# Kernel optimization log

Hardware: AMD Instinct MI355X
Metric: run time of the kernel (lower is better)

## Reference

```python
import jax, jax.numpy as jnp
import numpy as np

D_MODEL = 1024
NUM_HEADS = 16
HEAD_DIM = D_MODEL // NUM_HEADS


def setup_inputs() -> dict:
    key = jax.random.key(0)
    ks = jax.random.split(key, 11)
    B, S = 2, 2048
    s = 1.0 / np.sqrt(D_MODEL)
    inp = {
        "query": jax.random.normal(ks[0], (B, S, D_MODEL), jnp.float32),
        "key": jax.random.normal(ks[1], (B, S, D_MODEL), jnp.float32),
        "value": jax.random.normal(ks[2], (B, S, D_MODEL), jnp.float32),
        "Wq": jax.random.normal(ks[3], (D_MODEL, D_MODEL), jnp.float32) * s,
        "bq": jnp.zeros((D_MODEL,), jnp.float32),
        "Wk": jax.random.normal(ks[4], (D_MODEL, D_MODEL), jnp.float32) * s,
        "bk": jnp.zeros((D_MODEL,), jnp.float32),
        "Wv": jax.random.normal(ks[5], (D_MODEL, D_MODEL), jnp.float32) * s,
        "bv": jnp.zeros((D_MODEL,), jnp.float32),
        "Wo": jax.random.normal(ks[6], (D_MODEL, D_MODEL), jnp.float32) * s,
        "bo": jnp.zeros((D_MODEL,), jnp.float32),
    }
    return inp


def _split_heads(x):
    B, S, _ = x.shape
    return x.reshape(B, S, NUM_HEADS, HEAD_DIM).transpose(0, 2, 1, 3)  # [B,H,S,d]


def reference(query, key, value, Wq, bq, Wk, bk, Wv, bv, Wo, bo):
    Q = _split_heads(query @ Wq.T + bq)
    K = _split_heads(key @ Wk.T + bk)
    V = _split_heads(value @ Wv.T + bv)
    scale = 1.0 / jnp.sqrt(jnp.asarray(HEAD_DIM, jnp.float32))
    scores = jnp.einsum("bhqd,bhkd->bhqk", Q, K) * scale  # [B,H,S,S]
    weights = jax.nn.softmax(scores, axis=-1)
    attn = jnp.einsum("bhqk,bhkd->bhqd", weights, V)
    B, H, S, d = attn.shape
    attn = attn.transpose(0, 2, 1, 3).reshape(B, S, H * d)
    return attn @ Wo.T + bo
```

## Files before the change

### kernel.cpp

```cpp
#include <hip/hip_runtime.h>


typedef unsigned short u16;
typedef __attribute__((ext_vector_type(8))) short short8;
typedef __attribute__((ext_vector_type(4))) float floatx4;

__device__ __forceinline__ float bf2f(u16 x) {
  return __uint_as_float(((unsigned)x) << 16);
}
__device__ __forceinline__ u16 f2bf(float f) {
  unsigned x = __float_as_uint(f);
  return (u16)((x + 0x7fffu + ((x >> 16) & 1u)) >> 16);
}
__device__ __forceinline__ void gll16(const u16* g, u16* lds) {
  __builtin_amdgcn_global_load_lds((const __attribute__((address_space(1))) void*)g,
                                   (__attribute__((address_space(3))) void*)lds,
                                   16, 0, 0);
}

__global__ __launch_bounds__(256) void cvt_kernel(
    const float* __restrict__ q, const float* __restrict__ k, const float* __restrict__ v,
    const float* __restrict__ wq, const float* __restrict__ wk,
    const float* __restrict__ wv, const float* __restrict__ wo,
    const float* __restrict__ bq, const float* __restrict__ bk,
    const float* __restrict__ bv, const float* __restrict__ bo,
    u16* __restrict__ ws) {
  const int i4 = (blockIdx.x * 256 + threadIdx.x) * 4;
  const float* src;
  u16* dst;
  int local;
  if (i4 < 4194304)        { src = q;  dst = ws;            local = i4; }
  else if (i4 < 8388608)   { src = k;  dst = ws + 4194304;  local = i4 - 4194304; }
  else if (i4 < 12582912)  { src = v;  dst = ws + 8388608;  local = i4 - 8388608; }
  else if (i4 < 13631488)  { src = wq; dst = ws + 12582912; local = i4 - 12582912; }
  else if (i4 < 14680064)  { src = wk; dst = ws + 13631488; local = i4 - 13631488; }
  else if (i4 < 15728640)  { src = wv; dst = ws + 14680064; local = i4 - 14680064; }
  else if (i4 < 16777216)  { src = wo; dst = ws + 15728640; local = i4 - 15728640; }
  else if (i4 < 16778240)  { src = bq; dst = ws + 16777216; local = i4 - 16777216; }
  else if (i4 < 16779264)  { src = bk; dst = ws + 16779264; local = i4 - 16778240; }
  else if (i4 < 16780288)  { src = bv; dst = ws + 16781312; local = i4 - 16779264; }
  else                     { src = bo; dst = ws + 16783360; local = i4 - 16780288; }
  const float4 f = *(const float4*)(src + local);
  ushort4 o;
  o.x = f2bf(f.x); o.y = f2bf(f.y); o.z = f2bf(f.z); o.w = f2bf(f.w);
  *(ushort4*)(dst + local) = o;
}

__device__ __forceinline__ void gemm_tile(
    const u16* __restrict__ X, const u16* __restrict__ W,
    const u16* __restrict__ bias, u16* __restrict__ out16, float* __restrict__ out32,
    int row0, int col0, int mode, float oscale, u16* As, u16* Bs) {
  const int tid = threadIdx.x;
  const int w = tid >> 6, l = tid & 63;
  const int lan = l & 15, quad = l >> 4;
  const int wm = w & 1, wn = w >> 1;

  floatx4 acc[4][4];
#pragma unroll
  for (int i = 0; i < 4; ++i)
#pragma unroll
    for (int j = 0; j < 4; ++j) acc[i][j] = (floatx4)0.0f;

  const int r0 = tid >> 2, kq0 = tid & 3;
  const int r1 = (tid + 256) >> 2;
  u16* aB0 = As + w * 512;
  u16* aB1 = As + 2048 + w * 512;
  u16* bB0 = Bs + w * 512;
  u16* bB1 = Bs + 2048 + w * 512;
  const u16* Xa0 = X + (size_t)(row0 + r0) * 1024 + kq0 * 8;
  const u16* Xa1 = X + (size_t)(row0 + r1) * 1024 + kq0 * 8;
  const u16* Wb0 = W + (size_t)(col0 + r0) * 1024 + kq0 * 8;
  const u16* Wb1 = W + (size_t)(col0 + r1) * 1024 + kq0 * 8;

  for (int kt = 0; kt < 32; ++kt) {
    gll16(Xa0 + kt * 32, aB0);
    gll16(Xa1 + kt * 32, aB1);
    gll16(Wb0 + kt * 32, bB0);
    gll16(Wb1 + kt * 32, bB1);
    __syncthreads();

    short8 af[4], bfr[4];
#pragma unroll
    for (int i = 0; i < 4; ++i)
      af[i] = *(const short8*)(As + (wm * 64 + i * 16 + lan) * 32 + quad * 8);
#pragma unroll
    for (int j = 0; j < 4; ++j)
      bfr[j] = *(const short8*)(Bs + (wn * 64 + j * 16 + lan) * 32 + quad * 8);
#pragma unroll
    for (int i = 0; i < 4; ++i)
#pragma unroll
      for (int j = 0; j < 4; ++j)
        acc[i][j] = __builtin_amdgcn_mfma_f32_16x16x32_bf16(af[i], bfr[j], acc[i][j], 0, 0, 0);
    __syncthreads();
  }

#pragma unroll
  for (int i = 0; i < 4; ++i) {
    const int mb = row0 + wm * 64 + i * 16 + quad * 4;
#pragma unroll
    for (int j = 0; j < 4; ++j) {
      const int n = col0 + wn * 64 + j * 16 + lan;
      const float bv = bf2f(bias[n]);
      if (mode == 0) {
#pragma unroll
        for (int r = 0; r < 4; ++r)
          out16[(size_t)(mb + r) * 1024 + n] = f2bf((acc[i][j][r] + bv) * oscale);
      } else if (mode == 1) {
        const int b = mb >> 11, s = mb & 2047;
        const int h = n >> 6, dd = n & 63;
        ushort4 v;
        v.x = f2bf(acc[i][j][0] + bv);
        v.y = f2bf(acc[i][j][1] + bv);
        v.z = f2bf(acc[i][j][2] + bv);
        v.w = f2bf(acc[i][j][3] + bv);
        *(ushort4*)(out16 + (size_t)((b * 16 + h) * 64 + dd) * 2048 + s) = v;
      } else {
#pragma unroll
        for (int r = 0; r < 4; ++r)
          out32[(size_t)(mb + r) * 1024 + n] = acc[i][j][r] + bv;
      }
    }
  }
}

__global__ __launch_bounds__(256) void qkv_kernel(
    const u16* __restrict__ xq, const u16* __restrict__ xk, const u16* __restrict__ xv,
    const u16* __restrict__ Wq, const u16* __restrict__ Wk, const u16* __restrict__ Wv,
    const u16* __restrict__ bq, const u16* __restrict__ bk, const u16* __restrict__ bv,
    u16* __restrict__ Qo, u16* __restrict__ Ko, u16* __restrict__ Vto) {
  __shared__ __align__(16) u16 As[128 * 32];
  __shared__ __align__(16) u16 Bs[128 * 32];
  const int bx = blockIdx.x;
  const int tile_m = bx / 24;
  const int rem = bx - tile_m * 24;
  const int which = rem >> 3;
  const int col0 = (rem & 7) * 128;
  const u16* X = which == 0 ? xq : (which == 1 ? xk : xv);
  const u16* W = which == 0 ? Wq : (which == 1 ? Wk : Wv);
  const u16* bias = which == 0 ? bq : (which == 1 ? bk : bv);
  u16* out = which == 0 ? Qo : (which == 1 ? Ko : Vto);
  const float C = 0.125f * 1.4426950408889634f;
  gemm_tile(X, W, bias, out, nullptr, tile_m * 128, col0, which == 2 ? 1 : 0,
            which == 0 ? C : 1.0f, As, Bs);
}

__global__ __launch_bounds__(256) void proj_kernel(
    const u16* __restrict__ X, const u16* __restrict__ W,
    const u16* __restrict__ bias, float* __restrict__ out) {
  __shared__ __align__(16) u16 As[128 * 32];
  __shared__ __align__(16) u16 Bs[128 * 32];
  const int bx = blockIdx.x;
  gemm_tile(X, W, bias, nullptr, out, (bx >> 3) * 128, (bx & 7) * 128, 2, 1.0f, As, Bs);
}

#define PAD 72
#define FIXMAX 16.0f
__global__ __launch_bounds__(256, 4) void attn_kernel(
    const u16* __restrict__ Q, const u16* __restrict__ K,
    const u16* __restrict__ Vt, u16* __restrict__ O) {
  __shared__ __align__(16) u16 Qs[64 * PAD];
  __shared__ __align__(16) u16 Ks[64 * PAD];
  __shared__ __align__(16) u16 Vs[64 * PAD];
  __shared__ __align__(16) u16 Ps[64 * PAD];
  const int tid = threadIdx.x;
  const int w = tid >> 6, l = tid & 63;
  const int lan = l & 15, quad = l >> 4;
  const int q0 = blockIdx.x * 64;
  const int bh = blockIdx.y;
  const int b = bh >> 4, h = bh & 15;
  const u16* Qg = Q + (size_t)(b * 2048 + q0) * 1024 + h * 64;
  const u16* Kg = K + (size_t)(b * 2048) * 1024 + h * 64;
  const u16* Vg = Vt + (size_t)((b * 16 + h) * 64) * 2048;

  {
    const int c0 = tid, c1 = tid + 256;
    *(short8*)(Qs + (c0 >> 3) * PAD + (c0 & 7) * 8) =
        *(const short8*)(Qg + (size_t)(c0 >> 3) * 1024 + (c0 & 7) * 8);
    *(short8*)(Qs + (c1 >> 3) * PAD + (c1 & 7) * 8) =
        *(const short8*)(Qg + (size_t)(c1 >> 3) * 1024 + (c1 & 7) * 8);
  }
  __syncthreads();

  short8 aq[2];
#pragma unroll
  for (int kk = 0; kk < 2; ++kk)
    aq[kk] = *(const short8*)(Qs + (w * 16 + lan) * PAD + kk * 32 + quad * 8);

  float lrun[4];
  floatx4 oacc[4];
#pragma unroll
  for (int r = 0; r < 4; ++r) lrun[r] = 0.f;
#pragma unroll
  for (int nd = 0; nd < 4; ++nd) oacc[nd] = (floatx4)0.0f;

  const int rowA = tid >> 3, colq = tid & 7;
  const int rowB = (tid + 256) >> 3;

  short8 k0 = *(const short8*)(Kg + (size_t)rowA * 1024 + colq * 8);
  short8 k1 = *(const short8*)(Kg + (size_t)rowB * 1024 + colq * 8);
  short8 v0 = *(const short8*)(Vg + (size_t)rowA * 2048 + colq * 8);
  short8 v1 = *(const short8*)(Vg + (size_t)rowB * 2048 + colq * 8);

  for (int kt = 0; kt < 32; ++kt) {
    __syncthreads();
    *(short8*)(Ks + rowA * PAD + colq * 8) = k0;
    *(short8*)(Ks + rowB * PAD + colq * 8) = k1;
    *(short8*)(Vs + rowA * PAD + colq * 8) = v0;
    *(short8*)(Vs + rowB * PAD + colq * 8) = v1;
    __syncthreads();

    const int kn = kt < 31 ? kt + 1 : 31;
    k0 = *(const short8*)(Kg + (size_t)(kn * 64 + rowA) * 1024 + colq * 8);
    k1 = *(const short8*)(Kg + (size_t)(kn * 64 + rowB) * 1024 + colq * 8);
    v0 = *(const short8*)(Vg + (size_t)rowA * 2048 + kn * 64 + colq * 8);
    v1 = *(const short8*)(Vg + (size_t)rowB * 2048 + kn * 64 + colq * 8);

    short8 bkf[4][2], vb[4][2];
#pragma unroll
    for (int nj = 0; nj < 4; ++nj)
#pragma unroll
      for (int kk = 0; kk < 2; ++kk)
        bkf[nj][kk] = *(const short8*)(Ks + (nj * 16 + lan) * PAD + kk * 32 + quad * 8);
#pragma unroll
    for (int nd = 0; nd < 4; ++nd)
#pragma unroll
      for (int kk = 0; kk < 2; ++kk)
        vb[nd][kk] = *(const short8*)(Vs + (nd * 16 + lan) * PAD + kk * 32 + quad * 8);

    floatx4 sacc[4];
#pragma unroll
    for (int nj = 0; nj < 4; ++nj) sacc[nj] = (floatx4)(-FIXMAX);
#pragma unroll
    for (int kk = 0; kk < 2; ++kk)
#pragma unroll
      for (int nj = 0; nj < 4; ++nj)
        sacc[nj] = __builtin_amdgcn_mfma_f32_16x16x32_bf16(aq[kk], bkf[nj][kk], sacc[nj], 0, 0, 0);

#pragma unroll
    for (int r = 0; r < 4; ++r) {
      const float p0 = exp2f(sacc[0][r]), p1 = exp2f(sacc[1][r]);
      const float p2 = exp2f(sacc[2][r]), p3 = exp2f(sacc[3][r]);
      lrun[r] += (p0 + p1) + (p2 + p3);
      const int qrow = w * 16 + quad * 4 + r;
      Ps[qrow * PAD + lan] = f2bf(p0);
      Ps[qrow * PAD + 16 + lan] = f2bf(p1);
      Ps[qrow * PAD + 32 + lan] = f2bf(p2);
      Ps[qrow * PAD + 48 + lan] = f2bf(p3);
    }
    __threadfence_block();

    short8 pa[2];
#pragma unroll
    for (int kk = 0; kk < 2; ++kk)
      pa[kk] = *(const short8*)(Ps + (w * 16 + lan) * PAD + kk * 32 + quad * 8);
#pragma unroll
    for (int kk = 0; kk < 2; ++kk)
#pragma unroll
      for (int nd = 0; nd < 4; ++nd)
        oacc[nd] = __builtin_amdgcn_mfma_f32_16x16x32_bf16(pa[kk], vb[nd][kk], oacc[nd], 0, 0, 0);
  }

#pragma unroll
  for (int r = 0; r < 4; ++r) {
    float ls = lrun[r];
#pragma unroll
    for (int d = 1; d < 16; d <<= 1) ls += __shfl_xor(ls, d);
    const float inv = 1.0f / ls;
    const int mg = b * 2048 + q0 + w * 16 + quad * 4 + r;
#pragma unroll
    for (int nd = 0; nd < 4; ++nd) {
      const int col = h * 64 + nd * 16 + lan;
      O[(size_t)mg * 1024 + col] = f2bf(oacc[nd][r] * inv);
    }
  }
}

extern "C" void kernel_launch(void* const* d_in, const int* in_sizes, int n_in,
                              void* d_out, int out_size, void* d_ws, size_t ws_size,
                              hipStream_t stream) {
  const float* query = (const float*)d_in[0];
  const float* key_ = (const float*)d_in[1];
  const float* value = (const float*)d_in[2];
  const float* Wq = (const float*)d_in[3];
  const float* bq = (const float*)d_in[4];
  const float* Wk = (const float*)d_in[5];
  const float* bk = (const float*)d_in[6];
  const float* Wv = (const float*)d_in[7];
  const float* bv = (const float*)d_in[8];
  const float* Wo = (const float*)d_in[9];
  const float* bo = (const float*)d_in[10];
  float* out = (float*)d_out;

  u16* ws = (u16*)d_ws;
  u16* Xq = ws;
  u16* Xk = ws + 4194304;
  u16* Xv = ws + 8388608;
  u16* cWq = ws + 12582912;
  u16* cWk = ws + 13631488;
  u16* cWv = ws + 14680064;
  u16* cWo = ws + 15728640;
  u16* cbq = ws + 16777216;
  u16* cbk = ws + 16779264;
  u16* cbv = ws + 16781312;
  u16* cbo = ws + 16783360;
  u16* Qw = ws + 17301504;
  u16* Kw = ws + 21495808;
  u16* Vtw = ws + 25690112;
  u16* Ow = ws + 29884416;

  cvt_kernel<<<16388, 256, 0, stream>>>(query, key_, value, Wq, Wk, Wv, Wo,
                                        bq, bk, bv, bo, ws);
  qkv_kernel<<<768, 256, 0, stream>>>(Xq, Xk, Xv, cWq, cWk, cWv, cbq, cbk, cbv,
                                      Qw, Kw, Vtw);
  attn_kernel<<<dim3(32, 32), 256, 0, stream>>>(Qw, Kw, Vtw, Ow);
  proj_kernel<<<256, 256, 0, stream>>>(Ow, cWo, cbo, out);
}
```

Before: 270.0 us.

## Split attention key range across waves with per-wave LDS and cross-wave reduction

Each of the four waves now handles all 64 query rows against its own quarter of the keys, instead of each wave owning 16 query rows over all keys. K, V and P tiles live in per-wave LDS regions, so the block-wide barriers inside the loop become wave-local waitcnt fences. The row sums and output accumulators are reduced across waves through LDS at the end. This removes per-iteration block synchronisation and redundant K/V fragment loads, but it raises register use (occupancy hint lowered from 4 to 2) and adds an epilogue reduction.

```diff
diff --git a/kernel.cpp b/kernel.cpp
--- a/kernel.cpp
+++ b/kernel.cpp
@@ -17,6 +17,7 @@
                                    (__attribute__((address_space(3))) void*)lds,
                                    16, 0, 0);
 }
+#define DSFENCE() __asm__ volatile("s_waitcnt lgkmcnt(0)" ::: "memory")
 
 __global__ __launch_bounds__(256) void cvt_kernel(
     const float* __restrict__ q, const float* __restrict__ k, const float* __restrict__ v,
@@ -153,15 +154,12 @@
   gemm_tile(X, W, bias, nullptr, out, (bx >> 3) * 128, (bx & 7) * 128, 2, 1.0f, As, Bs);
 }
 
-#define PAD 72
 #define FIXMAX 16.0f
-__global__ __launch_bounds__(256, 4) void attn_kernel(
+__global__ __launch_bounds__(256, 2) void attn_kernel(
     const u16* __restrict__ Q, const u16* __restrict__ K,
     const u16* __restrict__ Vt, u16* __restrict__ O) {
-  __shared__ __align__(16) u16 Qs[64 * PAD];
-  __shared__ __align__(16) u16 Ks[64 * PAD];
-  __shared__ __align__(16) u16 Vs[64 * PAD];
-  __shared__ __align__(16) u16 Ps[64 * PAD];
+  __shared__ __align__(16) u16 lds[30208];
+  __shared__ float Lbuf[256];
   const int tid = threadIdx.x;
   const int w = tid >> 6, l = tid & 63;
   const int lan = l & 15, quad = l >> 4;
@@ -169,109 +167,134 @@
   const int bh = blockIdx.y;
   const int b = bh >> 4, h = bh & 15;
   const u16* Qg = Q + (size_t)(b * 2048 + q0) * 1024 + h * 64;
-  const u16* Kg = K + (size_t)(b * 2048) * 1024 + h * 64;
-  const u16* Vg = Vt + (size_t)((b * 16 + h) * 64) * 2048;
-
-  {
-    const int c0 = tid, c1 = tid + 256;
-    *(short8*)(Qs + (c0 >> 3) * PAD + (c0 & 7) * 8) =
-        *(const short8*)(Qg + (size_t)(c0 >> 3) * 1024 + (c0 & 7) * 8);
-    *(short8*)(Qs + (c1 >> 3) * PAD + (c1 & 7) * 8) =
-        *(const short8*)(Qg + (size_t)(c1 >> 3) * 1024 + (c1 & 7) * 8);
-  }
+  const u16* Kg = K + (size_t)(b * 2048 + w * 512) * 1024 + h * 64;
+  const u16* Vg = Vt + (size_t)((b * 16 + h) * 64) * 2048 + w * 512;
+  u16* Ksw = lds + w * 2304;
+  u16* Vsw = lds + 9216 + w * 2560;
+  u16* Psw = lds + 19456 + w * 2560;
+
+  short8 aq[4][2];
+#pragma unroll
+  for (int mi = 0; mi < 4; ++mi)
+#pragma unroll
+    for (int kk = 0; kk < 2; ++kk)
+      aq[mi][kk] = *(const short8*)(Qg + (size_t)(mi * 16 + lan) * 1024 + kk * 32 + quad * 8);
+
+  float lrun[4][4];
+  floatx4 oacc[4][4];
+#pragma unroll
+  for (int mi = 0; mi < 4; ++mi) {
+#pragma unroll
+    for (int r = 0; r < 4; ++r) lrun[mi][r] = 0.f;
+#pragma unroll
+    for (int nd = 0; nd < 4; ++nd) oacc[mi][nd] = (floatx4)0.0f;
+  }
+
+  const int krow = l >> 3, kcol = (l & 7) * 8;
+  const int vdd = l >> 2, vcol = (l & 3) * 8;
+
+  short8 kp[4], vp[4];
+#pragma unroll
+  for (int p = 0; p < 4; ++p) {
+    kp[p] = *(const short8*)(Kg + (size_t)(p * 8 + krow) * 1024 + kcol);
+    vp[p] = *(const short8*)(Vg + (size_t)(p * 16 + vdd) * 2048 + vcol);
+  }
+
+  for (int kt = 0; kt < 16; ++kt) {
+    DSFENCE();
+#pragma unroll
+    for (int p = 0; p < 4; ++p) {
+      *(short8*)(Ksw + (p * 8 + krow) * 72 + kcol) = kp[p];
+      *(short8*)(Vsw + (p * 16 + vdd) * 40 + vcol) = vp[p];
+    }
+    DSFENCE();
+
+    const int kn = kt < 15 ? kt + 1 : 15;
+#pragma unroll
+    for (int p = 0; p < 4; ++p) {
+      kp[p] = *(const short8*)(Kg + (size_t)(kn * 32 + p * 8 + krow) * 1024 + kcol);
+      vp[p] = *(const short8*)(Vg + (size_t)(p * 16 + vdd) * 2048 + kn * 32 + vcol);
+    }
+
+    short8 bkf[2][2];
+#pragma unroll
+    for (int nj = 0; nj < 2; ++nj)
+#pragma unroll
+      for (int kk = 0; kk < 2; ++kk)
+        bkf[nj][kk] = *(const short8*)(Ksw + (nj * 16 + lan) * 72 + kk * 32 + quad * 8);
+    floatx4 sacc[4][2];
+#pragma unroll
+    for (int mi = 0; mi < 4; ++mi)
+#pragma unroll
+      for (int nj = 0; nj < 2; ++nj) sacc[mi][nj] = (floatx4)(-FIXMAX);
+#pragma unroll
+    for (int kk = 0; kk < 2; ++kk)
+#pragma unroll
+      for (int mi = 0; mi < 4; ++mi)
+#pragma unroll
+        for (int nj = 0; nj < 2; ++nj)
+          sacc[mi][nj] =
+              __builtin_amdgcn_mfma_f32_16x16x32_bf16(aq[mi][kk], bkf[nj][kk], sacc[mi][nj], 0, 0, 0);
+
+#pragma unroll
+    for (int mi = 0; mi < 4; ++mi)
+#pragma unroll
+      for (int r = 0; r < 4; ++r) {
+        const float p0 = exp2f(sacc[mi][0][r]);
+        const float p1 = exp2f(sacc[mi][1][r]);
+        lrun[mi][r] += p0 + p1;
+        const int qrow = mi * 16 + quad * 4 + r;
+        Psw[qrow * 40 + lan] = f2bf(p0);
+        Psw[qrow * 40 + 16 + lan] = f2bf(p1);
+      }
+    DSFENCE();
+
+    short8 pa[4], vb[4];
+#pragma unroll
+    for (int mi = 0; mi < 4; ++mi)
+      pa[mi] = *(const short8*)(Psw + (mi * 16 + lan) * 40 + quad * 8);
+#pragma unroll
+    for (int nd = 0; nd < 4; ++nd)
+      vb[nd] = *(const short8*)(Vsw + (nd * 16 + lan) * 40 + quad * 8);
+#pragma unroll
+    for (int mi = 0; mi < 4; ++mi)
+#pragma unroll
+      for (int nd = 0; nd < 4; ++nd)
+        oacc[mi][nd] = __builtin_amdgcn_mfma_f32_16x16x32_bf16(pa[mi], vb[nd], oacc[mi][nd], 0, 0, 0);
+  }
+
+#pragma unroll
+  for (int mi = 0; mi < 4; ++mi)
+#pragma unroll
+    for (int r = 0; r < 4; ++r) {
+      float ls = lrun[mi][r];
+#pragma unroll
+      for (int d = 1; d < 16; d <<= 1) ls += __shfl_xor(ls, d);
+      if (lan == 0) Lbuf[w * 64 + mi * 16 + quad * 4 + r] = ls;
+    }
   __syncthreads();
-
-  short8 aq[2];
-#pragma unroll
-  for (int kk = 0; kk < 2; ++kk)
-    aq[kk] = *(const short8*)(Qs + (w * 16 + lan) * PAD + kk * 32 + quad * 8);
-
-  float lrun[4];
-  floatx4 oacc[4];
-#pragma unroll
-  for (int r = 0; r < 4; ++r) lrun[r] = 0.f;
-#pragma unroll
-  for (int nd = 0; nd < 4; ++nd) oacc[nd] = (floatx4)0.0f;
-
-  const int rowA = tid >> 3, colq = tid & 7;
-  const int rowB = (tid + 256) >> 3;
-
-  short8 k0 = *(const short8*)(Kg + (size_t)rowA * 1024 + colq * 8);
-  short8 k1 = *(const short8*)(Kg + (size_t)rowB * 1024 + colq * 8);
-  short8 v0 = *(const short8*)(Vg + (size_t)rowA * 2048 + colq * 8);
-  short8 v1 = *(const short8*)(Vg + (size_t)rowB * 2048 + colq * 8);
-
-  for (int kt = 0; kt < 32; ++kt) {
+  const int qm = tid >> 2, d0 = (tid & 3) * 4;
+  const float linv =
+      1.0f / (Lbuf[qm] + Lbuf[64 + qm] + Lbuf[128 + qm] + Lbuf[192 + qm]);
+  float* Obuf = (float*)(lds + 19456);
+
+#pragma unroll
+  for (int nd = 0; nd < 4; ++nd) {
     __syncthreads();
-    *(short8*)(Ks + rowA * PAD + colq * 8) = k0;
-    *(short8*)(Ks + rowB * PAD + colq * 8) = k1;
-    *(short8*)(Vs + rowA * PAD + colq * 8) = v0;
-    *(short8*)(Vs + rowB * PAD + colq * 8) = v1;
+#pragma unroll
+    for (int mi = 0; mi < 4; ++mi)
+#pragma unroll
+      for (int r = 0; r < 4; ++r)
+        Obuf[w * 1088 + (mi * 16 + quad * 4 + r) * 17 + lan] = oacc[mi][nd][r];
     __syncthreads();
-
-    const int kn = kt < 31 ? kt + 1 : 31;
-    k0 = *(const short8*)(Kg + (size_t)(kn * 64 + rowA) * 1024 + colq * 8);
-    k1 = *(const short8*)(Kg + (size_t)(kn * 64 + rowB) * 1024 + colq * 8);
-    v0 = *(const short8*)(Vg + (size_t)rowA * 2048 + kn * 64 + colq * 8);
-    v1 = *(const short8*)(Vg + (size_t)rowB * 2048 + kn * 64 + colq * 8);
-
-    short8 bkf[4][2], vb[4][2];
-#pragma unroll
-    for (int nj = 0; nj < 4; ++nj)
-#pragma unroll
-      for (int kk = 0; kk < 2; ++kk)
-        bkf[nj][kk] = *(const short8*)(Ks + (nj * 16 + lan) * PAD + kk * 32 + quad * 8);
-#pragma unroll
-    for (int nd = 0; nd < 4; ++nd)
-#pragma unroll
-      for (int kk = 0; kk < 2; ++kk)
-        vb[nd][kk] = *(const short8*)(Vs + (nd * 16 + lan) * PAD + kk * 32 + quad * 8);
-
-    floatx4 sacc[4];
-#pragma unroll
-    for (int nj = 0; nj < 4; ++nj) sacc[nj] = (floatx4)(-FIXMAX);
-#pragma unroll
-    for (int kk = 0; kk < 2; ++kk)
-#pragma unroll
-      for (int nj = 0; nj < 4; ++nj)
-        sacc[nj] = __builtin_amdgcn_mfma_f32_16x16x32_bf16(aq[kk], bkf[nj][kk], sacc[nj], 0, 0, 0);
-
-#pragma unroll
-    for (int r = 0; r < 4; ++r) {
-      const float p0 = exp2f(sacc[0][r]), p1 = exp2f(sacc[1][r]);
-      const float p2 = exp2f(sacc[2][r]), p3 = exp2f(sacc[3][r]);
-      lrun[r] += (p0 + p1) + (p2 + p3);
-      const int qrow = w * 16 + quad * 4 + r;
-      Ps[qrow * PAD + lan] = f2bf(p0);
-      Ps[qrow * PAD + 16 + lan] = f2bf(p1);
-      Ps[qrow * PAD + 32 + lan] = f2bf(p2);
-      Ps[qrow * PAD + 48 + lan] = f2bf(p3);
-    }
-    __threadfence_block();
-
-    short8 pa[2];
-#pragma unroll
-    for (int kk = 0; kk < 2; ++kk)
-      pa[kk] = *(const short8*)(Ps + (w * 16 + lan) * PAD + kk * 32 + quad * 8);
-#pragma unroll
-    for (int kk = 0; kk < 2; ++kk)
-#pragma unroll
-      for (int nd = 0; nd < 4; ++nd)
-        oacc[nd] = __builtin_amdgcn_mfma_f32_16x16x32_bf16(pa[kk], vb[nd][kk], oacc[nd], 0, 0, 0);
-  }
-
-#pragma unroll
-  for (int r = 0; r < 4; ++r) {
-    float ls = lrun[r];
-#pragma unroll
-    for (int d = 1; d < 16; d <<= 1) ls += __shfl_xor(ls, d);
-    const float inv = 1.0f / ls;
-    const int mg = b * 2048 + q0 + w * 16 + quad * 4 + r;
-#pragma unroll
-    for (int nd = 0; nd < 4; ++nd) {
-      const int col = h * 64 + nd * 16 + lan;
-      O[(size_t)mg * 1024 + col] = f2bf(oacc[nd][r] * inv);
-    }
+    ushort4 ov;
+#pragma unroll
+    for (int e = 0; e < 4; ++e) {
+      const float s = Obuf[qm * 17 + d0 + e] + Obuf[1088 + qm * 17 + d0 + e] +
+                      Obuf[2176 + qm * 17 + d0 + e] + Obuf[3264 + qm * 17 + d0 + e];
+      ((u16*)&ov)[e] = f2bf(s * linv);
+    }
+    *(ushort4*)(O + (size_t)(b * 2048 + q0 + qm) * 1024 + h * 64 + nd * 16 + d0) = ov;
   }
 }
 
```

New measurement: 273.1 us. Within noise of the previous version (+1.1%).

## Load V and Q fragments directly from global, drop their LDS staging

Applied to the files above, without the earlier changes.

The attention kernel now reads Q fragments and V^T MFMA operands straight from global memory into registers, so the Qs and Vs shared buffers and the V LDS store/load path are removed. K staging in LDS is kept. It also switches to a native exp2 builtin, packs bf16 conversions in pairs, replaces the block fence with an explicit lgkmcnt wait, and lowers the launch-bounds occupancy hint from 4 to 3. This cuts LDS traffic and footprint, but V reads become uncoalesced per-lane global loads issued without prefetch ahead of use, which adds latency.

```diff
diff --git a/kernel.cpp b/kernel.cpp
--- a/kernel.cpp
+++ b/kernel.cpp
@@ -1,4 +1,5 @@
 #include <hip/hip_runtime.h>
+#include <hip/hip_bf16.h>
 
 
 typedef unsigned short u16;
@@ -12,11 +13,23 @@
   unsigned x = __float_as_uint(f);
   return (u16)((x + 0x7fffu + ((x >> 16) & 1u)) >> 16);
 }
+__device__ __forceinline__ ushort2 pk_bf16(float a, float b) {
+  __hip_bfloat162 h2 = __float22bfloat162_rn(make_float2(a, b));
+  ushort2 u;
+  __builtin_memcpy(&u, &h2, 4);
+  return u;
+}
+#if __has_builtin(__builtin_amdgcn_exp2f)
+#define EXP2(x) __builtin_amdgcn_exp2f(x)
+#else
+#define EXP2(x) exp2f(x)
+#endif
 __device__ __forceinline__ void gll16(const u16* g, u16* lds) {
   __builtin_amdgcn_global_load_lds((const __attribute__((address_space(1))) void*)g,
                                    (__attribute__((address_space(3))) void*)lds,
                                    16, 0, 0);
 }
+#define DSFENCE() __asm__ volatile("s_waitcnt lgkmcnt(0)" ::: "memory")
 
 __global__ __launch_bounds__(256) void cvt_kernel(
     const float* __restrict__ q, const float* __restrict__ k, const float* __restrict__ v,
@@ -153,15 +166,14 @@
   gemm_tile(X, W, bias, nullptr, out, (bx >> 3) * 128, (bx & 7) * 128, 2, 1.0f, As, Bs);
 }
 
-#define PAD 72
 #define FIXMAX 16.0f
-__global__ __launch_bounds__(256, 4) void attn_kernel(
+#define KPAD 72
+__global__ __launch_bounds__(256, 3) void attn_kernel(
     const u16* __restrict__ Q, const u16* __restrict__ K,
     const u16* __restrict__ Vt, u16* __restrict__ O) {
-  __shared__ __align__(16) u16 Qs[64 * PAD];
-  __shared__ __align__(16) u16 Ks[64 * PAD];
-  __shared__ __align__(16) u16 Vs[64 * PAD];
-  __shared__ __align__(16) u16 Ps[64 * PAD];
+  __shared__ __align__(16) u16 Ks[64 * KPAD];
+  __shared__ __align__(16) u16 Ps[64 * KPAD];
+  __shared__ float Lbuf[64];
   const int tid = threadIdx.x;
   const int w = tid >> 6, l = tid & 63;
   const int lan = l & 15, quad = l >> 4;
@@ -171,20 +183,12 @@
   const u16* Qg = Q + (size_t)(b * 2048 + q0) * 1024 + h * 64;
   const u16* Kg = K + (size_t)(b * 2048) * 1024 + h * 64;
   const u16* Vg = Vt + (size_t)((b * 16 + h) * 64) * 2048;
-
-  {
-    const int c0 = tid, c1 = tid + 256;
-    *(short8*)(Qs + (c0 >> 3) * PAD + (c0 & 7) * 8) =
-        *(const short8*)(Qg + (size_t)(c0 >> 3) * 1024 + (c0 & 7) * 8);
-    *(short8*)(Qs + (c1 >> 3) * PAD + (c1 & 7) * 8) =
-        *(const short8*)(Qg + (size_t)(c1 >> 3) * 1024 + (c1 & 7) * 8);
-  }
-  __syncthreads();
+  (void)Lbuf;
 
   short8 aq[2];
 #pragma unroll
   for (int kk = 0; kk < 2; ++kk)
-    aq[kk] = *(const short8*)(Qs + (w * 16 + lan) * PAD + kk * 32 + quad * 8);
+    aq[kk] = *(const short8*)(Qg + (size_t)(w * 16 + lan) * 1024 + kk * 32 + quad * 8);
 
   float lrun[4];
   floatx4 oacc[4];
@@ -193,39 +197,36 @@
 #pragma unroll
   for (int nd = 0; nd < 4; ++nd) oacc[nd] = (floatx4)0.0f;
 
-  const int rowA = tid >> 3, colq = tid & 7;
-  const int rowB = (tid + 256) >> 3;
-
-  short8 k0 = *(const short8*)(Kg + (size_t)rowA * 1024 + colq * 8);
-  short8 k1 = *(const short8*)(Kg + (size_t)rowB * 1024 + colq * 8);
-  short8 v0 = *(const short8*)(Vg + (size_t)rowA * 2048 + colq * 8);
-  short8 v1 = *(const short8*)(Vg + (size_t)rowB * 2048 + colq * 8);
+  const int rowA = tid >> 3, colq = (tid & 7) * 8;
+  const int rowB = rowA + 32;
+
+  short8 k0 = *(const short8*)(Kg + (size_t)rowA * 1024 + colq);
+  short8 k1 = *(const short8*)(Kg + (size_t)rowB * 1024 + colq);
 
   for (int kt = 0; kt < 32; ++kt) {
     __syncthreads();
-    *(short8*)(Ks + rowA * PAD + colq * 8) = k0;
-    *(short8*)(Ks + rowB * PAD + colq * 8) = k1;
-    *(short8*)(Vs + rowA * PAD + colq * 8) = v0;
-    *(short8*)(Vs + rowB * PAD + colq * 8) = v1;
+    *(short8*)(Ks + rowA * KPAD + colq) = k0;
+    *(short8*)(Ks + rowB * KPAD + colq) = k1;
     __syncthreads();
 
     const int kn = kt < 31 ? kt + 1 : 31;
-    k0 = *(const short8*)(Kg + (size_t)(kn * 64 + rowA) * 1024 + colq * 8);
-    k1 = *(const short8*)(Kg + (size_t)(kn * 64 + rowB) * 1024 + colq * 8);
-    v0 = *(const short8*)(Vg + (size_t)rowA * 2048 + kn * 64 + colq * 8);
-    v1 = *(const short8*)(Vg + (size_t)rowB * 2048 + kn * 64 + colq * 8);
-
-    short8 bkf[4][2], vb[4][2];
+    k0 = *(const short8*)(Kg + (size_t)(kn * 64 + rowA) * 1024 + colq);
+    k1 = *(const short8*)(Kg + (size_t)(kn * 64 + rowB) * 1024 + colq);
+
+    short8 vb[4][2];
+#pragma unroll
+    for (int nd = 0; nd < 4; ++nd)
+#pragma unroll
+      for (int kk = 0; kk < 2; ++kk)
+        vb[nd][kk] = *(const short8*)(Vg + (size_t)(nd * 16 + lan) * 2048 + kt * 64 +
+                                      kk * 32 + quad * 8);
+
+    short8 bkf[4][2];
 #pragma unroll
     for (int nj = 0; nj < 4; ++nj)
 #pragma unroll
       for (int kk = 0; kk < 2; ++kk)
-        bkf[nj][kk] = *(const short8*)(Ks + (nj * 16 + lan) * PAD + kk * 32 + quad * 8);
-#pragma unroll
-    for (int nd = 0; nd < 4; ++nd)
-#pragma unroll
-      for (int kk = 0; kk < 2; ++kk)
-        vb[nd][kk] = *(const short8*)(Vs + (nd * 16 + lan) * PAD + kk * 32 + quad * 8);
+        bkf[nj][kk] = *(const short8*)(Ks + (nj * 16 + lan) * KPAD + kk * 32 + quad * 8);
 
     floatx4 sacc[4];
 #pragma unroll
@@ -238,21 +239,23 @@
 
 #pragma unroll
     for (int r = 0; r < 4; ++r) {
-      const float p0 = exp2f(sacc[0][r]), p1 = exp2f(sacc[1][r]);
-      const float p2 = exp2f(sacc[2][r]), p3 = exp2f(sacc[3][r]);
+      const float p0 = EXP2(sacc[0][r]), p1 = EXP2(sacc[1][r]);
+      const float p2 = EXP2(sacc[2][r]), p3 = EXP2(sacc[3][r]);
       lrun[r] += (p0 + p1) + (p2 + p3);
+      const ushort2 pa01 = pk_bf16(p0, p1);
+      const ushort2 pa23 = pk_bf16(p2, p3);
       const int qrow = w * 16 + quad * 4 + r;
-      Ps[qrow * PAD + lan] = f2bf(p0);
-      Ps[qrow * PAD + 16 + lan] = f2bf(p1);
-      Ps[qrow * PAD + 32 + lan] = f2bf(p2);
-      Ps[qrow * PAD + 48 + lan] = f2bf(p3);
+      Ps[qrow * KPAD + lan] = pa01.x;
+      Ps[qrow * KPAD + 16 + lan] = pa01.y;
+      Ps[qrow * KPAD + 32 + lan] = pa23.x;
+      Ps[qrow * KPAD + 48 + lan] = pa23.y;
     }
-    __threadfence_block();
+    DSFENCE();
 
     short8 pa[2];
 #pragma unroll
     for (int kk = 0; kk < 2; ++kk)
-      pa[kk] = *(const short8*)(Ps + (w * 16 + lan) * PAD + kk * 32 + quad * 8);
+      pa[kk] = *(const short8*)(Ps + (w * 16 + lan) * KPAD + kk * 32 + quad * 8);
 #pragma unroll
     for (int kk = 0; kk < 2; ++kk)
 #pragma unroll
```

Result: slower. 323.8 us (+19.9%).
